# Kernel tuning notes

Hardware: AMD Instinct MI355X
Metric: run time of the kernel (lower is better)

## Reference

```python
import jax, jax.numpy as jnp
import numpy as np

B, T, E, H = 8, 1024, 1024, 16
D = E // H  # per-head dim = 64


def setup_inputs() -> dict:
    key = jax.random.key(0)
    ks = jax.random.split(key, 10)
    s = 0.05
    return {
        "source": jax.random.normal(ks[0], (B, T, E), jnp.float32),
        "target": jax.random.normal(ks[1], (B, T, E), jnp.float32),
        "W_q": jax.random.normal(ks[2], (1, H, D, D), jnp.float32) * s,
        "W_v": jax.random.normal(ks[3], (1, H, D, D), jnp.float32) * s,
        "W_o": jax.random.normal(ks[4], (1, H, D, D), jnp.float32) * s,
        "W_ih": jax.random.normal(ks[5], (H, D, D), jnp.float32) * s,
        "W_hh": jax.random.normal(ks[6], (H, D, D), jnp.float32) * s,
        "b_ih": jax.random.normal(ks[7], (H, D), jnp.float32) * s,
        "b_hh": jax.random.normal(ks[8], (H, D), jnp.float32) * s,
    }


def reference(source, target, W_q, W_v, W_o, W_ih, W_hh, b_ih, b_hh):
    b, t, e = source.shape
    h = W_ih.shape[0]
    d = e // h
    # split heads: [B, H, T, d]
    q = source.reshape(b, t, h, d).transpose(0, 2, 1, 3)
    k = target.reshape(b, t, h, d).transpose(0, 2, 1, 3)
    v = k
    # per-head projections (grammar path: k is NOT projected)
    q = jnp.einsum('bhtd,hde->bhte', q, W_q[0])
    v = jnp.einsum('bhtd,hde->bhte', v, W_v[0])
    # RNN positional key generation (per head, batch_first nn.RNN, tanh).
    # step 0: input = k[:, :, 0, :], hidden = 0  ->  h1 = tanh(x @ Wih^T + b_ih + b_hh)
    k0 = k[:, :, 0, :]  # [B, H, d]
    h1 = jnp.tanh(jnp.einsum('bhd,hed->bhe', k0, W_ih) + b_ih + b_hh)
    # steps t>=1: next_word fed back as BOTH input and hidden state
    def step(hs, _):
        hn = jnp.tanh(jnp.einsum('bhd,hed->bhe', hs, W_ih) + b_ih
                      + jnp.einsum('bhd,hed->bhe', hs, W_hh) + b_hh)
        return hn, hn
    _, rest = jax.lax.scan(step, h1, None, length=t - 1)  # [T-1, B, H, d]
    nw = jnp.concatenate([h1[None], rest], axis=0).transpose(1, 2, 0, 3)  # [B,H,T,d]
    # scores / sqrt(d)  (time_attention), then merge_attn divides by sqrt(T)
    scores = jnp.einsum('bhqd,bhkd->bhqk', q, nw) / float(np.sqrt(d))
    w = jax.nn.softmax(scores / float(np.sqrt(t)), axis=-1)
    out = jnp.einsum('bhqk,bhkd->bhqd', w, v)
    out = jnp.einsum('bhtd,hde->bhte', out, W_o[0])
    return out.transpose(0, 2, 1, 3).reshape(b, t, e)
```

## Files before the change

kernel.cpp:

```cpp
#include <hip/hip_runtime.h>

typedef unsigned short u16;
typedef short short8 __attribute__((ext_vector_type(8)));
typedef float f32x4 __attribute__((ext_vector_type(4)));
typedef _Float16 f16;
typedef f16 f16x2 __attribute__((ext_vector_type(2)));
typedef f16 f16x8 __attribute__((ext_vector_type(8)));

#define B_ 8
#define T_ 1024
#define E_ 1024
#define H_ 16
#define D_ 64
#define BH_ 128

__device__ __forceinline__ float ftanh(float x){
    x = fminf(8.0f, fmaxf(-8.0f, x));
    float e2 = __expf(2.0f * x);
    return 1.0f - 2.0f * __builtin_amdgcn_rcpf(e2 + 1.0f);
}

__device__ __forceinline__ u16 f2h(float x){
    union { f16 h; u16 u; } v; v.h = (f16)x; return v.u;
}

__device__ __forceinline__ float dot8(f16x8 a, f16x8 b, float acc){
#if __has_builtin(__builtin_amdgcn_fdot2)
    f16x2 a0 = {a[0],a[1]}, a1 = {a[2],a[3]}, a2 = {a[4],a[5]}, a3 = {a[6],a[7]};
    f16x2 b0 = {b[0],b[1]}, b1 = {b[2],b[3]}, b2 = {b[4],b[5]}, b3 = {b[6],b[7]};
    acc = __builtin_amdgcn_fdot2(a0, b0, acc, false);
    acc = __builtin_amdgcn_fdot2(a1, b1, acc, false);
    acc = __builtin_amdgcn_fdot2(a2, b2, acc, false);
    acc = __builtin_amdgcn_fdot2(a3, b3, acc, false);
#else
    #pragma unroll
    for (int i = 0; i < 8; ++i) acc += (float)a[i] * (float)b[i];
#endif
    return acc;
}

__device__ __forceinline__ f16x8 pack8(f32x4 a, f32x4 b){
    f16x8 r;
    r[0]=(f16)a[0]; r[1]=(f16)a[1]; r[2]=(f16)a[2]; r[3]=(f16)a[3];
    r[4]=(f16)b[0]; r[5]=(f16)b[1]; r[6]=(f16)b[2]; r[7]=(f16)b[3];
    return r;
}

#define PIN8(x) do { f32x4 _t = __builtin_bit_cast(f32x4, x); \
                     asm volatile("" : "+v"(_t));             \
                     x = __builtin_bit_cast(f16x8, _t); } while (0)

__global__ __launch_bounds__(256, 1) void proj_rnn_kernel(
    const float* __restrict__ src, const float* __restrict__ tgt,
    const float* __restrict__ Wq,  const float* __restrict__ Wv,
    const float* __restrict__ Wih, const float* __restrict__ Whh,
    const float* __restrict__ bih, const float* __restrict__ bhh,
    u16* __restrict__ qh, u16* __restrict__ vh, u16* __restrict__ nwh)
{
    int bid = blockIdx.x;
    if (bid < BH_) {
        if (threadIdx.x >= 64) return;
        __shared__ __align__(16) u16 hl[D_];
        const int b = bid >> 4, h = bid & 15;
        const int e = threadIdx.x;

        const f32x4* wi4 = (const f32x4*)(Wih + ((size_t)h * D_ + e) * D_);
        const f32x4* wh4 = (const f32x4*)(Whh + ((size_t)h * D_ + e) * D_);
        float c = bih[h * D_ + e] + bhh[h * D_ + e];
        asm volatile("" : "+v"(c));

        f16x8 n0 = pack8(wi4[0],  wi4[1]),  n1 = pack8(wi4[2],  wi4[3]);
        f16x8 n2 = pack8(wi4[4],  wi4[5]),  n3 = pack8(wi4[6],  wi4[7]);
        f16x8 n4 = pack8(wi4[8],  wi4[9]),  n5 = pack8(wi4[10], wi4[11]);
        f16x8 n6 = pack8(wi4[12], wi4[13]), n7 = pack8(wi4[14], wi4[15]);
        f16x8 m0 = pack8(wi4[0]+wh4[0],   wi4[1]+wh4[1]);
        f16x8 m1 = pack8(wi4[2]+wh4[2],   wi4[3]+wh4[3]);
        f16x8 m2 = pack8(wi4[4]+wh4[4],   wi4[5]+wh4[5]);
        f16x8 m3 = pack8(wi4[6]+wh4[6],   wi4[7]+wh4[7]);
        f16x8 m4 = pack8(wi4[8]+wh4[8],   wi4[9]+wh4[9]);
        f16x8 m5 = pack8(wi4[10]+wh4[10], wi4[11]+wh4[11]);
        f16x8 m6 = pack8(wi4[12]+wh4[12], wi4[13]+wh4[13]);
        f16x8 m7 = pack8(wi4[14]+wh4[14], wi4[15]+wh4[15]);
        PIN8(m0); PIN8(m1); PIN8(m2); PIN8(m3);
        PIN8(m4); PIN8(m5); PIN8(m6); PIN8(m7);

        hl[e] = f2h(tgt[(size_t)b * T_ * E_ + h * D_ + e]);

        u16* nwp = nwh + (size_t)bid * T_ * D_;
        const f16x8* hl8 = (const f16x8*)hl;

        {
            f16x8 x0=hl8[0],x1=hl8[1],x2=hl8[2],x3=hl8[3],
                  x4=hl8[4],x5=hl8[5],x6=hl8[6],x7=hl8[7];
            float s0=dot8(n0,x0,c),   s1=dot8(n1,x1,0.f),
                  s2=dot8(n2,x2,0.f), s3=dot8(n3,x3,0.f),
                  s4=dot8(n4,x4,0.f), s5=dot8(n5,x5,0.f),
                  s6=dot8(n6,x6,0.f), s7=dot8(n7,x7,0.f);
            float hv = ftanh(((s0+s1)+(s2+s3)) + ((s4+s5)+(s6+s7)));
            u16 hb = f2h(hv);
            hl[e] = hb;
            nwp[e] = hb;
        }

        #pragma unroll 1
        for (int t = 1; t < T_; ++t) {
            f16x8 x0=hl8[0],x1=hl8[1],x2=hl8[2],x3=hl8[3],
                  x4=hl8[4],x5=hl8[5],x6=hl8[6],x7=hl8[7];
            float s0=dot8(m0,x0,c),   s1=dot8(m1,x1,0.f),
                  s2=dot8(m2,x2,0.f), s3=dot8(m3,x3,0.f),
                  s4=dot8(m4,x4,0.f), s5=dot8(m5,x5,0.f),
                  s6=dot8(m6,x6,0.f), s7=dot8(m7,x7,0.f);
            float hv = ftanh(((s0+s1)+(s2+s3)) + ((s4+s5)+(s6+s7)));
            u16 hb = f2h(hv);
            hl[e] = hb;
            nwp[(size_t)t * D_ + e] = hb;
        }
    } else {
        int pb   = bid - BH_;
        int bh   = pb >> 5;
        int tile = pb & 31;
        int b = bh >> 4, h = bh & 15;
        int e  = threadIdx.x & 63;
        int tg = threadIdx.x >> 6;
        int t0 = tile * 32 + tg * 8;

        const float* wq = Wq + (size_t)h * D_ * D_ + e;
        const float* wv = Wv + (size_t)h * D_ * D_ + e;
        const float* s0 = src + ((size_t)b * T_ + t0) * E_ + h * D_;
        const float* g0 = tgt + ((size_t)b * T_ + t0) * E_ + h * D_;

        float aq[8] = {0,0,0,0,0,0,0,0};
        float av[8] = {0,0,0,0,0,0,0,0};
        #pragma unroll 4
        for (int d4 = 0; d4 < 16; ++d4) {
            float q0 = wq[(4*d4+0)*64], q1 = wq[(4*d4+1)*64],
                  q2 = wq[(4*d4+2)*64], q3 = wq[(4*d4+3)*64];
            float v0 = wv[(4*d4+0)*64], v1 = wv[(4*d4+1)*64],
                  v2 = wv[(4*d4+2)*64], v3 = wv[(4*d4+3)*64];
            #pragma unroll
            for (int j = 0; j < 8; ++j) {
                float4 x = *(const float4*)(s0 + (size_t)j * E_ + 4*d4);
                float4 y = *(const float4*)(g0 + (size_t)j * E_ + 4*d4);
                aq[j] += x.x*q0 + x.y*q1 + x.z*q2 + x.w*q3;
                av[j] += y.x*v0 + y.y*v1 + y.z*v2 + y.w*v3;
            }
        }
        u16* qp = qh + ((size_t)bh * T_ + t0) * D_ + e;
        #pragma unroll
        for (int j = 0; j < 8; ++j) qp[(size_t)j * D_] = f2h(aq[j] * (1.0f/256.0f));
        f16x8 vv;
        #pragma unroll
        for (int j = 0; j < 8; ++j) vv[j] = (f16)av[j];
        *(f16x8*)(vh + ((size_t)bh * D_ + e) * T_ + t0) = vv;
    }
}

#define MFMA16(a, b, c) __builtin_amdgcn_mfma_f32_16x16x32_f16(a, b, c, 0, 0, 0)

__global__ __launch_bounds__(256) void attn_kernel(
    const u16* __restrict__ qh,
    const u16* __restrict__ kh,
    const u16* __restrict__ vh,
    const float* __restrict__ Wo,
    float* __restrict__ out)
{
    __shared__ __align__(16) u16 Klds[64 * 64];
    __shared__ __align__(16) u16 Vlds[64 * 64];
    __shared__ __align__(16) u16 Plds[4][16 * 64];

    const int tid  = threadIdx.x;
    const int lane = tid & 63;
    const int w    = tid >> 6;
    const int l15  = lane & 15;
    const int quad = lane >> 4;
    const int sw   = lane & 7;
    const int bh   = blockIdx.y;
    const int qt   = blockIdx.x;

    const size_t base  = (size_t)bh * T_ * D_;
    const size_t vbase = (size_t)bh * D_ * T_;

    f16x8 aq0, aq1;
    {
        int qrow = qt * 64 + w * 16 + l15;
        const f16x8* qp = (const f16x8*)(qh + base + (size_t)qrow * 64 + quad * 8);
        aq0 = qp[0];
        aq1 = qp[4];
    }

    f32x4 oacc[4];
    #pragma unroll
    for (int i = 0; i < 4; ++i) oacc[i] = (f32x4){0.f, 0.f, 0.f, 0.f};
    float lrun[4] = {0.f, 0.f, 0.f, 0.f};

    u16* Pw = Plds[w];

    #pragma unroll 1
    for (int kt = 0; kt < 16; ++kt) {
        #pragma unroll
        for (int i = 0; i < 2; ++i) {
            int ch = tid + 256 * i;
            int r = ch >> 3, cc = ch & 7;
            short8 kval = *(const short8*)(kh + base + (size_t)(kt * 64 + r) * 64 + cc * 8);
            *(short8*)&Klds[r * 64 + ((cc ^ (r & 7)) * 8)] = kval;
            short8 vval = *(const short8*)(vh + vbase + (size_t)r * T_ + kt * 64 + cc * 8);
            *(short8*)&Vlds[r * 64 + ((cc ^ (r & 7)) * 8)] = vval;
        }
        __syncthreads();

        f32x4 sacc[4];
        #pragma unroll
        for (int u = 0; u < 4; ++u) {
            sacc[u] = (f32x4){0.f, 0.f, 0.f, 0.f};
            int row = 16 * u + l15;
            f16x8 bk0 = *(const f16x8*)&Klds[row * 64 + (((quad + 0) ^ sw) * 8)];
            f16x8 bk1 = *(const f16x8*)&Klds[row * 64 + (((quad + 4) ^ sw) * 8)];
            sacc[u] = MFMA16(aq0, bk0, sacc[u]);
            sacc[u] = MFMA16(aq1, bk1, sacc[u]);
        }

        float pr[4][4];
        #pragma unroll
        for (int r = 0; r < 4; ++r) {
            float rs = 0.f;
            #pragma unroll
            for (int u = 0; u < 4; ++u) {
                float pv = __expf(sacc[u][r]);
                pr[u][r] = pv;
                rs += pv;
            }
            #pragma unroll
            for (int off = 1; off < 16; off <<= 1)
                rs += __shfl_xor(rs, off, 16);
            lrun[r] += rs;
        }

        #pragma unroll
        for (int u = 0; u < 4; ++u) {
            int col = 16 * u + l15;
            #pragma unroll
            for (int r = 0; r < 4; ++r) {
                int row = quad * 4 + r;
                Pw[row * 64 + (((col >> 3) ^ (row & 7)) * 8) + (col & 7)] = f2h(pr[u][r]);
            }
        }

        #pragma unroll
        for (int kc = 0; kc < 2; ++kc) {
            f16x8 ap = *(const f16x8*)&Pw[l15 * 64 + (((quad + 4 * kc) ^ sw) * 8)];
            #pragma unroll
            for (int nt = 0; nt < 4; ++nt) {
                int drow = 16 * nt + l15;
                f16x8 bv = *(const f16x8*)&Vlds[drow * 64 + (((quad + 4 * kc) ^ sw) * 8)];
                oacc[nt] = MFMA16(ap, bv, oacc[nt]);
            }
        }
        __syncthreads();
    }

    const int b  = bh >> 4, hh = bh & 15;
    {
        const float* wo = Wo + (size_t)hh * D_ * D_;
        #pragma unroll
        for (int i = 0; i < 2; ++i) {
            int ch = tid + 256 * i;
            int e = ch >> 3, dc = ch & 7;
            short8 vch;
            #pragma unroll
            for (int j = 0; j < 8; ++j)
                vch[j] = (short)f2h(wo[(size_t)(dc * 8 + j) * D_ + e]);
            *(short8*)&Klds[e * 64 + ((dc ^ (e & 7)) * 8)] = vch;
        }
    }
    #pragma unroll
    for (int nt = 0; nt < 4; ++nt) {
        int col = 16 * nt + l15;
        #pragma unroll
        for (int r = 0; r < 4; ++r) {
            int row = quad * 4 + r;
            Pw[row * 64 + (((col >> 3) ^ (row & 7)) * 8) + (col & 7)] =
                f2h(oacc[nt][r] / lrun[r]);
        }
    }
    __syncthreads();

    f16x8 ao0 = *(const f16x8*)&Pw[l15 * 64 + (((quad + 0) ^ sw) * 8)];
    f16x8 ao1 = *(const f16x8*)&Pw[l15 * 64 + (((quad + 4) ^ sw) * 8)];
    f32x4 oo[4];
    #pragma unroll
    for (int nt = 0; nt < 4; ++nt) {
        oo[nt] = (f32x4){0.f, 0.f, 0.f, 0.f};
        int erow = 16 * nt + l15;
        f16x8 b0 = *(const f16x8*)&Klds[erow * 64 + (((quad + 0) ^ (erow & 7)) * 8)];
        f16x8 b1 = *(const f16x8*)&Klds[erow * 64 + (((quad + 4) ^ (erow & 7)) * 8)];
        oo[nt] = MFMA16(ao0, b0, oo[nt]);
        oo[nt] = MFMA16(ao1, b1, oo[nt]);
    }
    #pragma unroll
    for (int nt = 0; nt < 4; ++nt) {
        #pragma unroll
        for (int r = 0; r < 4; ++r) {
            int qg = qt * 64 + w * 16 + quad * 4 + r;
            int e  = 16 * nt + l15;
            out[((size_t)b * T_ + qg) * E_ + hh * D_ + e] = oo[nt][r];
        }
    }
}

extern "C" void kernel_launch(void* const* d_in, const int* in_sizes, int n_in,
                              void* d_out, int out_size, void* d_ws, size_t ws_size,
                              hipStream_t stream)
{
    const float* src = (const float*)d_in[0];
    const float* tgt = (const float*)d_in[1];
    const float* Wq  = (const float*)d_in[2];
    const float* Wv  = (const float*)d_in[3];
    const float* Wo  = (const float*)d_in[4];
    const float* Wih = (const float*)d_in[5];
    const float* Whh = (const float*)d_in[6];
    const float* bih = (const float*)d_in[7];
    const float* bhh = (const float*)d_in[8];
    float* out = (float*)d_out;

    char* ws = (char*)d_ws;
    u16* qh  = (u16*)(ws);
    u16* vh  = (u16*)(ws + (size_t)16 * 1024 * 1024);
    u16* nwh = (u16*)(ws + (size_t)32 * 1024 * 1024);

    (void)in_sizes; (void)n_in; (void)out_size; (void)ws_size;

    proj_rnn_kernel<<<dim3(BH_ + 4096), 256, 0, stream>>>(
        src, tgt, Wq, Wv, Wih, Whh, bih, bhh, qh, vh, nwh);
    attn_kernel<<<dim3(16, BH_), 256, 0, stream>>>(qh, nwh, vh, Wo, out);
}
```

Measured before the change: 397.3 us.

## Interleave two RNN chains per wave and restructure attention to register-fed MFMA

The RNN phase now runs two (batch, head) recurrences per wave, interleaving their dot products to hide the latency of the serial chain, and uses 64 blocks instead of 128. The attention kernel drops the shared-memory K/V staging and barriers, loads K and V fragments straight from global into registers, and gives each wave two 16-row query fragments (128 queries per block) with launch bounds set for 3 blocks per CU. The W_o transpose to fp16 moves into extra blocks of the first kernel. These changes target the serial recurrence latency and the per-tile LDS staging and barriers, at the cost of more registers and K/V reads from global memory.

```diff
diff --git a/kernel.cpp b/kernel.cpp
--- a/kernel.cpp
+++ b/kernel.cpp
@@ -5,6 +5,7 @@
 typedef float f32x4 __attribute__((ext_vector_type(4)));
 typedef _Float16 f16;
 typedef f16 f16x2 __attribute__((ext_vector_type(2)));
+typedef f16 f16x4 __attribute__((ext_vector_type(4)));
 typedef f16 f16x8 __attribute__((ext_vector_type(8)));
 
 #define B_ 8
@@ -13,6 +14,9 @@
 #define H_ 16
 #define D_ 64
 #define BH_ 128
+#define RNNB 64
+#define PROJB 4096
+#define WOB 16
 
 __device__ __forceinline__ float ftanh(float x){
     x = fminf(8.0f, fmaxf(-8.0f, x));
@@ -50,73 +54,103 @@
                      asm volatile("" : "+v"(_t));             \
                      x = __builtin_bit_cast(f16x8, _t); } while (0)
 
+#define PACKM(M, wi, wh) \
+    f16x8 M##0 = pack8(wi[0]+wh[0],   wi[1]+wh[1]);   \
+    f16x8 M##1 = pack8(wi[2]+wh[2],   wi[3]+wh[3]);   \
+    f16x8 M##2 = pack8(wi[4]+wh[4],   wi[5]+wh[5]);   \
+    f16x8 M##3 = pack8(wi[6]+wh[6],   wi[7]+wh[7]);   \
+    f16x8 M##4 = pack8(wi[8]+wh[8],   wi[9]+wh[9]);   \
+    f16x8 M##5 = pack8(wi[10]+wh[10], wi[11]+wh[11]); \
+    f16x8 M##6 = pack8(wi[12]+wh[12], wi[13]+wh[13]); \
+    f16x8 M##7 = pack8(wi[14]+wh[14], wi[15]+wh[15]);
+
+#define PACKN(N, wi) \
+    f16x8 N##0 = pack8(wi[0],  wi[1]);  \
+    f16x8 N##1 = pack8(wi[2],  wi[3]);  \
+    f16x8 N##2 = pack8(wi[4],  wi[5]);  \
+    f16x8 N##3 = pack8(wi[6],  wi[7]);  \
+    f16x8 N##4 = pack8(wi[8],  wi[9]);  \
+    f16x8 N##5 = pack8(wi[10], wi[11]); \
+    f16x8 N##6 = pack8(wi[12], wi[13]); \
+    f16x8 N##7 = pack8(wi[14], wi[15]);
+
+#define LOADX(X, hp) \
+    f16x8 X##0 = hp[0], X##1 = hp[1], X##2 = hp[2], X##3 = hp[3], \
+          X##4 = hp[4], X##5 = hp[5], X##6 = hp[6], X##7 = hp[7];
+
+#define DOT64(M, X, CC) \
+    ( ((dot8(M##0,X##0,CC) + dot8(M##1,X##1,0.f)) +   \
+       (dot8(M##2,X##2,0.f) + dot8(M##3,X##3,0.f))) + \
+      ((dot8(M##4,X##4,0.f) + dot8(M##5,X##5,0.f)) +  \
+       (dot8(M##6,X##6,0.f) + dot8(M##7,X##7,0.f))) )
+
 __global__ __launch_bounds__(256, 1) void proj_rnn_kernel(
     const float* __restrict__ src, const float* __restrict__ tgt,
     const float* __restrict__ Wq,  const float* __restrict__ Wv,
-    const float* __restrict__ Wih, const float* __restrict__ Whh,
-    const float* __restrict__ bih, const float* __restrict__ bhh,
-    u16* __restrict__ qh, u16* __restrict__ vh, u16* __restrict__ nwh)
+    const float* __restrict__ Wo,  const float* __restrict__ Wih,
+    const float* __restrict__ Whh, const float* __restrict__ bih,
+    const float* __restrict__ bhh,
+    u16* __restrict__ qh, u16* __restrict__ vh, u16* __restrict__ nwh,
+    u16* __restrict__ woT)
 {
     int bid = blockIdx.x;
-    if (bid < BH_) {
+    if (bid < RNNB) {
         if (threadIdx.x >= 64) return;
-        __shared__ __align__(16) u16 hl[D_];
-        const int b = bid >> 4, h = bid & 15;
+        __shared__ __align__(16) u16 hl[2][D_];
         const int e = threadIdx.x;
-
-        const f32x4* wi4 = (const f32x4*)(Wih + ((size_t)h * D_ + e) * D_);
-        const f32x4* wh4 = (const f32x4*)(Whh + ((size_t)h * D_ + e) * D_);
-        float c = bih[h * D_ + e] + bhh[h * D_ + e];
-        asm volatile("" : "+v"(c));
-
-        f16x8 n0 = pack8(wi4[0],  wi4[1]),  n1 = pack8(wi4[2],  wi4[3]);
-        f16x8 n2 = pack8(wi4[4],  wi4[5]),  n3 = pack8(wi4[6],  wi4[7]);
-        f16x8 n4 = pack8(wi4[8],  wi4[9]),  n5 = pack8(wi4[10], wi4[11]);
-        f16x8 n6 = pack8(wi4[12], wi4[13]), n7 = pack8(wi4[14], wi4[15]);
-        f16x8 m0 = pack8(wi4[0]+wh4[0],   wi4[1]+wh4[1]);
-        f16x8 m1 = pack8(wi4[2]+wh4[2],   wi4[3]+wh4[3]);
-        f16x8 m2 = pack8(wi4[4]+wh4[4],   wi4[5]+wh4[5]);
-        f16x8 m3 = pack8(wi4[6]+wh4[6],   wi4[7]+wh4[7]);
-        f16x8 m4 = pack8(wi4[8]+wh4[8],   wi4[9]+wh4[9]);
-        f16x8 m5 = pack8(wi4[10]+wh4[10], wi4[11]+wh4[11]);
-        f16x8 m6 = pack8(wi4[12]+wh4[12], wi4[13]+wh4[13]);
-        f16x8 m7 = pack8(wi4[14]+wh4[14], wi4[15]+wh4[15]);
-        PIN8(m0); PIN8(m1); PIN8(m2); PIN8(m3);
-        PIN8(m4); PIN8(m5); PIN8(m6); PIN8(m7);
-
-        hl[e] = f2h(tgt[(size_t)b * T_ * E_ + h * D_ + e]);
-
-        u16* nwp = nwh + (size_t)bid * T_ * D_;
-        const f16x8* hl8 = (const f16x8*)hl;
+        const int c0 = bid * 2, c1 = c0 + 1;
+        const int b0 = c0 >> 4, h0 = c0 & 15;
+        const int b1 = c1 >> 4, h1 = c1 & 15;
+        const f32x4* wiA = (const f32x4*)(Wih + ((size_t)h0 * D_ + e) * D_);
+        const f32x4* whA = (const f32x4*)(Whh + ((size_t)h0 * D_ + e) * D_);
+        const f32x4* wiB = (const f32x4*)(Wih + ((size_t)h1 * D_ + e) * D_);
+        const f32x4* whB = (const f32x4*)(Whh + ((size_t)h1 * D_ + e) * D_);
+        float cA = bih[h0 * D_ + e] + bhh[h0 * D_ + e];
+        float cB = bih[h1 * D_ + e] + bhh[h1 * D_ + e];
+        asm volatile("" : "+v"(cA));
+        asm volatile("" : "+v"(cB));
+
+        PACKM(mA, wiA, whA)
+        PACKM(mB, wiB, whB)
+        PIN8(mA0); PIN8(mA1); PIN8(mA2); PIN8(mA3);
+        PIN8(mA4); PIN8(mA5); PIN8(mA6); PIN8(mA7);
+        PIN8(mB0); PIN8(mB1); PIN8(mB2); PIN8(mB3);
+        PIN8(mB4); PIN8(mB5); PIN8(mB6); PIN8(mB7);
+
+        hl[0][e] = f2h(tgt[(size_t)b0 * T_ * E_ + h0 * D_ + e]);
+        hl[1][e] = f2h(tgt[(size_t)b1 * T_ * E_ + h1 * D_ + e]);
+
+        u16* npA = nwh + (size_t)c0 * T_ * D_;
+        u16* npB = nwh + (size_t)c1 * T_ * D_;
+        const f16x8* hA = (const f16x8*)hl[0];
+        const f16x8* hB = (const f16x8*)hl[1];
 
         {
-            f16x8 x0=hl8[0],x1=hl8[1],x2=hl8[2],x3=hl8[3],
-                  x4=hl8[4],x5=hl8[5],x6=hl8[6],x7=hl8[7];
-            float s0=dot8(n0,x0,c),   s1=dot8(n1,x1,0.f),
-                  s2=dot8(n2,x2,0.f), s3=dot8(n3,x3,0.f),
-                  s4=dot8(n4,x4,0.f), s5=dot8(n5,x5,0.f),
-                  s6=dot8(n6,x6,0.f), s7=dot8(n7,x7,0.f);
-            float hv = ftanh(((s0+s1)+(s2+s3)) + ((s4+s5)+(s6+s7)));
-            u16 hb = f2h(hv);
-            hl[e] = hb;
-            nwp[e] = hb;
+            PACKN(nA, wiA)
+            LOADX(xA, hA)
+            float hv = ftanh(DOT64(nA, xA, cA));
+            u16 hb = f2h(hv); hl[0][e] = hb; npA[e] = hb;
+        }
+        {
+            PACKN(nB, wiB)
+            LOADX(xB, hB)
+            float hv = ftanh(DOT64(nB, xB, cB));
+            u16 hb = f2h(hv); hl[1][e] = hb; npB[e] = hb;
         }
 
         #pragma unroll 1
         for (int t = 1; t < T_; ++t) {
-            f16x8 x0=hl8[0],x1=hl8[1],x2=hl8[2],x3=hl8[3],
-                  x4=hl8[4],x5=hl8[5],x6=hl8[6],x7=hl8[7];
-            float s0=dot8(m0,x0,c),   s1=dot8(m1,x1,0.f),
-                  s2=dot8(m2,x2,0.f), s3=dot8(m3,x3,0.f),
-                  s4=dot8(m4,x4,0.f), s5=dot8(m5,x5,0.f),
-                  s6=dot8(m6,x6,0.f), s7=dot8(m7,x7,0.f);
-            float hv = ftanh(((s0+s1)+(s2+s3)) + ((s4+s5)+(s6+s7)));
-            u16 hb = f2h(hv);
-            hl[e] = hb;
-            nwp[(size_t)t * D_ + e] = hb;
-        }
-    } else {
-        int pb   = bid - BH_;
+            LOADX(xA, hA)
+            LOADX(xB, hB)
+            float sA = DOT64(mA, xA, cA);
+            float sB = DOT64(mB, xB, cB);
+            float vA = ftanh(sA), vB = ftanh(sB);
+            u16 ua = f2h(vA), ub = f2h(vB);
+            hl[0][e] = ua; npA[(size_t)t * D_ + e] = ua;
+            hl[1][e] = ub; npB[(size_t)t * D_ + e] = ub;
+        }
+    } else if (bid < RNNB + PROJB) {
+        int pb   = bid - RNNB;
         int bh   = pb >> 5;
         int tile = pb & 31;
         int b = bh >> 4, h = bh & 15;
@@ -152,21 +186,30 @@
         #pragma unroll
         for (int j = 0; j < 8; ++j) vv[j] = (f16)av[j];
         *(f16x8*)(vh + ((size_t)bh * D_ + e) * T_ + t0) = vv;
+    } else {
+        int h = bid - (RNNB + PROJB);
+        const float* wsrc = Wo + (size_t)h * 4096;
+        u16* wdst = woT + (size_t)h * 4096;
+        int d  = threadIdx.x & 63;
+        int e0 = threadIdx.x >> 6;
+        #pragma unroll
+        for (int i = 0; i < 16; ++i) {
+            int e = e0 * 16 + i;
+            wdst[e * 64 + d] = f2h(wsrc[d * 64 + e]);
+        }
     }
 }
 
 #define MFMA16(a, b, c) __builtin_amdgcn_mfma_f32_16x16x32_f16(a, b, c, 0, 0, 0)
 
-__global__ __launch_bounds__(256) void attn_kernel(
+__global__ __launch_bounds__(256, 3) void attn_kernel(
     const u16* __restrict__ qh,
     const u16* __restrict__ kh,
     const u16* __restrict__ vh,
-    const float* __restrict__ Wo,
+    const u16* __restrict__ woT,
     float* __restrict__ out)
 {
-    __shared__ __align__(16) u16 Klds[64 * 64];
-    __shared__ __align__(16) u16 Vlds[64 * 64];
-    __shared__ __align__(16) u16 Plds[4][16 * 64];
+    __shared__ __align__(16) u16 Pl[4][2][16 * 64];
 
     const int tid  = threadIdx.x;
     const int lane = tid & 63;
@@ -174,135 +217,127 @@
     const int l15  = lane & 15;
     const int quad = lane >> 4;
     const int sw   = lane & 7;
-    const int bh   = blockIdx.y;
-    const int qt   = blockIdx.x;
+    const int bh   = blockIdx.x >> 3;
+    const int qblk = blockIdx.x & 7;
+    const int b    = bh >> 4, h = bh & 15;
 
     const size_t base  = (size_t)bh * T_ * D_;
     const size_t vbase = (size_t)bh * D_ * T_;
-
-    f16x8 aq0, aq1;
-    {
-        int qrow = qt * 64 + w * 16 + l15;
-        const f16x8* qp = (const f16x8*)(qh + base + (size_t)qrow * 64 + quad * 8);
-        aq0 = qp[0];
-        aq1 = qp[4];
-    }
-
-    f32x4 oacc[4];
-    #pragma unroll
-    for (int i = 0; i < 4; ++i) oacc[i] = (f32x4){0.f, 0.f, 0.f, 0.f};
-    float lrun[4] = {0.f, 0.f, 0.f, 0.f};
-
-    u16* Pw = Plds[w];
+    const int qbase = qblk * 128 + w * 32;
+
+    f16x8 aq[2][2];
+    #pragma unroll
+    for (int qf = 0; qf < 2; ++qf)
+        #pragma unroll
+        for (int kc = 0; kc < 2; ++kc)
+            aq[qf][kc] = *(const f16x8*)(qh + base +
+                (size_t)(qbase + qf*16 + l15) * 64 + kc*32 + quad*8);
+
+    f32x4 oacc[2][4];
+    #pragma unroll
+    for (int qf = 0; qf < 2; ++qf)
+        #pragma unroll
+        for (int nt = 0; nt < 4; ++nt) oacc[qf][nt] = (f32x4){0.f,0.f,0.f,0.f};
+    float lsum[2] = {0.f, 0.f};
+
+    u16* P0 = Pl[w][0];
+    u16* P1 = Pl[w][1];
+    const f32x4 zf = {0.f, 0.f, 0.f, 0.f};
 
     #pragma unroll 1
     for (int kt = 0; kt < 16; ++kt) {
-        #pragma unroll
-        for (int i = 0; i < 2; ++i) {
-            int ch = tid + 256 * i;
-            int r = ch >> 3, cc = ch & 7;
-            short8 kval = *(const short8*)(kh + base + (size_t)(kt * 64 + r) * 64 + cc * 8);
-            *(short8*)&Klds[r * 64 + ((cc ^ (r & 7)) * 8)] = kval;
-            short8 vval = *(const short8*)(vh + vbase + (size_t)r * T_ + kt * 64 + cc * 8);
-            *(short8*)&Vlds[r * 64 + ((cc ^ (r & 7)) * 8)] = vval;
-        }
-        __syncthreads();
-
-        f32x4 sacc[4];
-        #pragma unroll
-        for (int u = 0; u < 4; ++u) {
-            sacc[u] = (f32x4){0.f, 0.f, 0.f, 0.f};
-            int row = 16 * u + l15;
-            f16x8 bk0 = *(const f16x8*)&Klds[row * 64 + (((quad + 0) ^ sw) * 8)];
-            f16x8 bk1 = *(const f16x8*)&Klds[row * 64 + (((quad + 4) ^ sw) * 8)];
-            sacc[u] = MFMA16(aq0, bk0, sacc[u]);
-            sacc[u] = MFMA16(aq1, bk1, sacc[u]);
-        }
-
-        float pr[4][4];
-        #pragma unroll
-        for (int r = 0; r < 4; ++r) {
-            float rs = 0.f;
+        const u16* kp = kh + base + (size_t)(kt * 64) * 64;
+        f16x8 ka[4][2];
+        #pragma unroll
+        for (int u = 0; u < 4; ++u)
+            #pragma unroll
+            for (int kc = 0; kc < 2; ++kc)
+                ka[u][kc] = *(const f16x8*)(kp + (16*u + l15)*64 + kc*32 + quad*8);
+
+        #pragma unroll
+        for (int qf = 0; qf < 2; ++qf) {
+            u16* Pq = qf ? P1 : P0;
             #pragma unroll
             for (int u = 0; u < 4; ++u) {
-                float pv = __expf(sacc[u][r]);
-                pr[u][r] = pv;
-                rs += pv;
-            }
-            #pragma unroll
-            for (int off = 1; off < 16; off <<= 1)
-                rs += __shfl_xor(rs, off, 16);
-            lrun[r] += rs;
-        }
-
-        #pragma unroll
-        for (int u = 0; u < 4; ++u) {
-            int col = 16 * u + l15;
+                f32x4 st = MFMA16(ka[u][0], aq[qf][0], zf);
+                st       = MFMA16(ka[u][1], aq[qf][1], st);
+                float p0 = __expf(st[0]), p1 = __expf(st[1]),
+                      p2 = __expf(st[2]), p3 = __expf(st[3]);
+                lsum[qf] += (p0 + p1) + (p2 + p3);
+                f16x4 pk = {(f16)p0, (f16)p1, (f16)p2, (f16)p3};
+                int chunk = 2*u + (quad >> 1);
+                *(f16x4*)&Pq[l15*64 + ((chunk ^ sw) * 8) + (quad & 1) * 4] = pk;
+            }
+        }
+
+        f16x8 bv[4][2];
+        #pragma unroll
+        for (int nt = 0; nt < 4; ++nt)
+            #pragma unroll
+            for (int kc = 0; kc < 2; ++kc)
+                bv[nt][kc] = *(const f16x8*)(vh + vbase +
+                    (size_t)(16*nt + l15) * T_ + kt*64 + kc*32 + quad*8);
+
+        #pragma unroll
+        for (int qf = 0; qf < 2; ++qf) {
+            u16* Pq = qf ? P1 : P0;
+            f16x8 ap0 = *(const f16x8*)&Pq[l15*64 + (((0 + quad) ^ sw) * 8)];
+            f16x8 ap1 = *(const f16x8*)&Pq[l15*64 + (((4 + quad) ^ sw) * 8)];
+            #pragma unroll
+            for (int nt = 0; nt < 4; ++nt) {
+                oacc[qf][nt] = MFMA16(ap0, bv[nt][0], oacc[qf][nt]);
+                oacc[qf][nt] = MFMA16(ap1, bv[nt][1], oacc[qf][nt]);
+            }
+        }
+    }
+
+    float rl[2][4];
+    #pragma unroll
+    for (int qf = 0; qf < 2; ++qf) {
+        float l = lsum[qf];
+        l += __shfl_xor(l, 16, 64);
+        l += __shfl_xor(l, 32, 64);
+        #pragma unroll
+        for (int r = 0; r < 4; ++r)
+            rl[qf][r] = __builtin_amdgcn_rcpf(__shfl(l, quad*4 + r, 64));
+    }
+
+    #pragma unroll
+    for (int qf = 0; qf < 2; ++qf) {
+        u16* Pq = qf ? P1 : P0;
+        #pragma unroll
+        for (int nt = 0; nt < 4; ++nt) {
             #pragma unroll
             for (int r = 0; r < 4; ++r) {
-                int row = quad * 4 + r;
-                Pw[row * 64 + (((col >> 3) ^ (row & 7)) * 8) + (col & 7)] = f2h(pr[u][r]);
-            }
-        }
-
-        #pragma unroll
-        for (int kc = 0; kc < 2; ++kc) {
-            f16x8 ap = *(const f16x8*)&Pw[l15 * 64 + (((quad + 4 * kc) ^ sw) * 8)];
-            #pragma unroll
-            for (int nt = 0; nt < 4; ++nt) {
-                int drow = 16 * nt + l15;
-                f16x8 bv = *(const f16x8*)&Vlds[drow * 64 + (((quad + 4 * kc) ^ sw) * 8)];
-                oacc[nt] = MFMA16(ap, bv, oacc[nt]);
-            }
-        }
-        __syncthreads();
-    }
-
-    const int b  = bh >> 4, hh = bh & 15;
-    {
-        const float* wo = Wo + (size_t)hh * D_ * D_;
-        #pragma unroll
-        for (int i = 0; i < 2; ++i) {
-            int ch = tid + 256 * i;
-            int e = ch >> 3, dc = ch & 7;
-            short8 vch;
-            #pragma unroll
-            for (int j = 0; j < 8; ++j)
-                vch[j] = (short)f2h(wo[(size_t)(dc * 8 + j) * D_ + e]);
-            *(short8*)&Klds[e * 64 + ((dc ^ (e & 7)) * 8)] = vch;
-        }
-    }
-    #pragma unroll
-    for (int nt = 0; nt < 4; ++nt) {
-        int col = 16 * nt + l15;
-        #pragma unroll
-        for (int r = 0; r < 4; ++r) {
-            int row = quad * 4 + r;
-            Pw[row * 64 + (((col >> 3) ^ (row & 7)) * 8) + (col & 7)] =
-                f2h(oacc[nt][r] / lrun[r]);
-        }
-    }
-    __syncthreads();
-
-    f16x8 ao0 = *(const f16x8*)&Pw[l15 * 64 + (((quad + 0) ^ sw) * 8)];
-    f16x8 ao1 = *(const f16x8*)&Pw[l15 * 64 + (((quad + 4) ^ sw) * 8)];
-    f32x4 oo[4];
-    #pragma unroll
-    for (int nt = 0; nt < 4; ++nt) {
-        oo[nt] = (f32x4){0.f, 0.f, 0.f, 0.f};
-        int erow = 16 * nt + l15;
-        f16x8 b0 = *(const f16x8*)&Klds[erow * 64 + (((quad + 0) ^ (erow & 7)) * 8)];
-        f16x8 b1 = *(const f16x8*)&Klds[erow * 64 + (((quad + 4) ^ (erow & 7)) * 8)];
-        oo[nt] = MFMA16(ao0, b0, oo[nt]);
-        oo[nt] = MFMA16(ao1, b1, oo[nt]);
-    }
-    #pragma unroll
-    for (int nt = 0; nt < 4; ++nt) {
-        #pragma unroll
-        for (int r = 0; r < 4; ++r) {
-            int qg = qt * 64 + w * 16 + quad * 4 + r;
-            int e  = 16 * nt + l15;
-            out[((size_t)b * T_ + qg) * E_ + hh * D_ + e] = oo[nt][r];
+                int row = quad*4 + r, col = 16*nt + l15;
+                Pq[row*64 + (((col >> 3) ^ (row & 7)) * 8) + (col & 7)] =
+                    f2h(oacc[qf][nt][r] * rl[qf][r]);
+            }
+        }
+    }
+
+    f16x8 bw[4][2];
+    #pragma unroll
+    for (int nt = 0; nt < 4; ++nt)
+        #pragma unroll
+        for (int kc = 0; kc < 2; ++kc)
+            bw[nt][kc] = *(const f16x8*)(woT + (size_t)h*4096 +
+                (16*nt + l15)*64 + kc*32 + quad*8);
+
+    #pragma unroll
+    for (int qf = 0; qf < 2; ++qf) {
+        u16* Pq = qf ? P1 : P0;
+        f16x8 ao0 = *(const f16x8*)&Pq[l15*64 + (((0 + quad) ^ sw) * 8)];
+        f16x8 ao1 = *(const f16x8*)&Pq[l15*64 + (((4 + quad) ^ sw) * 8)];
+        #pragma unroll
+        for (int nt = 0; nt < 4; ++nt) {
+            f32x4 oo = MFMA16(ao0, bw[nt][0], zf);
+            oo       = MFMA16(ao1, bw[nt][1], oo);
+            #pragma unroll
+            for (int r = 0; r < 4; ++r) {
+                int qg = qbase + qf*16 + quad*4 + r;
+                out[((size_t)b * T_ + qg) * E_ + h*64 + 16*nt + l15] = oo[r];
+            }
         }
     }
 }
@@ -326,10 +361,11 @@
     u16* qh  = (u16*)(ws);
     u16* vh  = (u16*)(ws + (size_t)16 * 1024 * 1024);
     u16* nwh = (u16*)(ws + (size_t)32 * 1024 * 1024);
+    u16* woT = (u16*)(ws + (size_t)48 * 1024 * 1024);
 
     (void)in_sizes; (void)n_in; (void)out_size; (void)ws_size;
 
-    proj_rnn_kernel<<<dim3(BH_ + 4096), 256, 0, stream>>>(
-        src, tgt, Wq, Wv, Wih, Whh, bih, bhh, qh, vh, nwh);
-    attn_kernel<<<dim3(16, BH_), 256, 0, stream>>>(qh, nwh, vh, Wo, out);
-}
+    proj_rnn_kernel<<<dim3(RNNB + PROJB + WOB), 256, 0, stream>>>(
+        src, tgt, Wq, Wv, Wo, Wih, Whh, bih, bhh, qh, vh, nwh, woT);
+    attn_kernel<<<dim3(8 * BH_), 256, 0, stream>>>(qh, nwh, vh, woT, out);
+}
```

Result: slower. 551.6 us (+38.9%).
